# Optimization experiments

Measured on AMD Instinct MI355X. Metric: run time of the kernel, lower is better.

## Reference

```python
import jax, jax.numpy as jnp
import numpy as np

NEMBED, EMBED_DIM, HID_DIM, OUT_DIM, NUM_CLASSES = 128, 64, 128, 128, 2
BATCH, TEAM = 2048, 5
N_OPS = 8


def setup_inputs() -> dict:
    key = jax.random.key(0)
    ks = jax.random.split(key, 8)
    w_eq = np.sqrt(2.0 / (EMBED_DIM + HID_DIM + N_OPS))
    return {
        "x": jax.random.randint(ks[0], (BATCH, 2, TEAM), 0, NEMBED, dtype=jnp.int32),
        "embed": jax.random.normal(ks[1], (NEMBED, EMBED_DIM), jnp.float32) * 0.1,
        "coefs1": jax.random.normal(ks[2], (EMBED_DIM, HID_DIM, N_OPS), jnp.float32) * w_eq,
        "bias1": jnp.zeros((HID_DIM,), jnp.float32),
        "wout1": jax.random.normal(ks[3], (HID_DIM, OUT_DIM), jnp.float32) * np.sqrt(1.0 / HID_DIM),
        "bout1": jnp.zeros((OUT_DIM,), jnp.float32),
        "coefs2": jax.random.normal(ks[4], (EMBED_DIM, HID_DIM, N_OPS), jnp.float32) * w_eq,
        "bias2": jnp.zeros((HID_DIM,), jnp.float32),
        "wout2": jax.random.normal(ks[5], (HID_DIM, OUT_DIM), jnp.float32) * np.sqrt(1.0 / HID_DIM),
        "bout2": jnp.zeros((OUT_DIM,), jnp.float32),
        "fcw": jax.random.normal(ks[6], (2 * OUT_DIM, NCLS := NUM_CLASSES and 2 * OUT_DIM and NUM_CLASSES), jnp.float32) * np.sqrt(1.0 / (2 * OUT_DIM)),
        "fcb": jnp.zeros((NUM_CLASSES,), jnp.float32),
    }


def eset_ops_3_to_3(t):
    # t: (N, D, m, m, m). 8 equivariant basis ops: keep-or-(sum&broadcast) each axis.
    # Pooled ops are kept with singleton dims; broadcasting happens after the
    # channel contraction (cheaper, same math as expand-then-contract).
    s1 = t.sum(-3, keepdims=True)
    s2 = t.sum(-2, keepdims=True)
    s3 = t.sum(-1, keepdims=True)
    s12 = t.sum((-3, -2), keepdims=True)
    s13 = t.sum((-3, -1), keepdims=True)
    s23 = t.sum((-2, -1), keepdims=True)
    sall = t.sum((-3, -2, -1), keepdims=True)
    return [t, s1, s2, s3, s12, s13, s23, sall]


def eq3_layer(t, coefs, bias):
    # coefs: (D_in, D_out, 8); output (N, D_out, m, m, m)
    ops = eset_ops_3_to_3(t)
    out = 0.0
    for b, op in enumerate(ops):
        out = out + jnp.einsum('ndijk,ds->nsijk', op, coefs[:, :, b])
    return out + bias[None, :, None, None, None]


def setnet3to3(t, coefs, bias, wout, bout):
    h = jax.nn.relu(eq3_layer(t, coefs, bias))          # (N, H, m, m, m)
    return jnp.einsum('nsijk,so->nijko', h, wout) + bout  # (N, m, m, m, out_dim)


def reference(x, embed, coefs1, bias1, wout1, bout1, coefs2, bias2, wout2, bout2, fcw, fcb):
    e1 = jax.nn.relu(embed[x[:, 0]])  # (N, 5, D)
    e2 = jax.nn.relu(embed[x[:, 1]])
    t1 = jnp.einsum('bid,bjd,bkd->bdijk', e1, e1, e1)  # (N, D, 5, 5, 5)
    t2 = jnp.einsum('bid,bjd,bkd->bdijk', e2, e2, e2)
    o1 = setnet3to3(t1, coefs1, bias1, wout1, bout1)
    o2 = setnet3to3(t2, coefs2, bias2, wout2, bout2)
    t1e = jax.nn.relu(o1.mean(axis=(1, 2, 3)))  # (N, out_dim)
    t2e = jax.nn.relu(o2.mean(axis=(1, 2, 3)))
    z = jnp.concatenate([t1e, t2e], axis=-1)    # dropout_prob=0 / eval mode: no-op
    return z @ fcw + fcb
```

## Files before the change

### kernel.cpp

```cpp
#include <hip/hip_runtime.h>


typedef __attribute__((ext_vector_type(8))) short bf16x8;
typedef __attribute__((ext_vector_type(4))) float f32x4;
typedef __attribute__((ext_vector_type(4))) unsigned u32x4;

#define DEV __device__ __forceinline__
#define MFMA __builtin_amdgcn_mfma_f32_16x16x32_bf16

DEV constexpr int pid2(int a, int b) {
  int x = a < b ? a : b, y = a < b ? b : a;
  return x * (9 - x) / 2 + y;
}
DEV constexpr int tid3(int i, int j, int k) {
  int a = i, b = j, c = k, t;
  if (a > b) { t = a; a = b; b = t; }
  if (b > c) { t = b; b = c; c = t; }
  if (a > b) { t = a; a = b; b = t; }
  return a * (a * a - 18 * a + 107) / 6 + (b - a) * (11 - a - b) / 2 + (c - b);
}
DEV ushort f2bf(float f) {
  unsigned u = __builtin_bit_cast(unsigned, f);
  return (ushort)((u + 0x7FFFu + ((u >> 16) & 1u)) >> 16);
}
DEV unsigned pk2(float a, float b) {
  return (unsigned)f2bf(a) | ((unsigned)f2bf(b) << 16);
}

__global__ __launch_bounds__(256)
void prep_kernel(const float* __restrict__ c1, const float* __restrict__ c2,
                 const float* __restrict__ w1, const float* __restrict__ w2,
                 ushort* __restrict__ ctf, float* __restrict__ wt, int do_wt) {
  const int idx = blockIdx.x * 256 + threadIdx.x;
  if (idx < 131072) {
    const int e = idx & 7, l = (idx >> 3) & 63, nt = (idx >> 9) & 7,
              kt = (idx >> 12) & 1, bank = (idx >> 13) & 7, side = (idx >> 16) & 1;
    const int d = 32 * kt + 8 * (l >> 4) + e;
    const int s = 16 * nt + (l & 15);
    ctf[idx] = f2bf((side ? c2 : c1)[(d * 128 + s) * 8 + bank]);
  } else if (do_wt) {
    const int j = idx - 131072;
    if (j < 65536) {
      const int s = j & 127, o = (j >> 7) & 127, side = j >> 14;
      wt[j] = (side ? w2 : w1)[s * 128 + o] * (1.f / 125.f);
    }
  }
}

__global__ __launch_bounds__(256, 3)
void eq3_wavegemm(const int* __restrict__ x, const float* __restrict__ embed,
                  const float* __restrict__ bias1, const float* __restrict__ bias2,
                  const float* __restrict__ bout1, const float* __restrict__ bout2,
                  const float* __restrict__ wout1, const float* __restrict__ wout2,
                  const float* __restrict__ fcw,
                  const ushort* __restrict__ ctf, const float* __restrict__ wt,
                  float* __restrict__ pbuf, int nunits)
{
  __shared__ ushort FT[80 * 64];
  __shared__ ushort TS[8 * 2184];
  __shared__ float  S2[256];
  __shared__ float  SW[256];
  __shared__ float  fcp[4];

  const int tid = threadIdx.x;
  const int w = tid >> 6, l = tid & 63, grp = l >> 4, lc = l & 15;

  for (int e = tid; e < 24 * 64; e += 256) {
    const int r = e >> 6, d = e & 63;
    const int row = (r < 13) ? 35 + r : ((r == 13) ? 63 : 70 + (r - 14));
    FT[(row * 64 + d) ^ ((row & 7) << 3)] = 0;
  }
  int uprev = -1;

  for (int u = blockIdx.x; u < nunits; u += gridDim.x) {
    const int side = u & 1;

    {
      const int d = tid & 63, q = tid >> 6;
      const int* xn = x + u * 5;
      float v[5];
      #pragma unroll
      for (int i = 0; i < 5; ++i) v[i] = fmaxf(embed[xn[i] * 64 + d], 0.f);
      const float Sv = v[0] + v[1] + v[2] + v[3] + v[4];
      const float Sq = Sv * Sv, Sc = Sq * Sv;
      float p2a[15];
      {
        int c2 = 0;
        #pragma unroll
        for (int a = 0; a < 5; ++a)
          #pragma unroll
          for (int b = a; b < 5; ++b) { p2a[c2] = v[a] * v[b]; ++c2; }
      }
      {
        int c3 = 0;
        #pragma unroll
        for (int a = 0; a < 5; ++a)
          #pragma unroll
          for (int b = a; b < 5; ++b)
            #pragma unroll
            for (int c = b; c < 5; ++c) {
              const int qq = (c3 < 14) ? 0 : ((c3 < 28) ? 1 : 2);
              if (q == qq)
                FT[(c3 * 64 + d) ^ ((c3 & 7) << 3)] = f2bf(p2a[pid2(a, b)] * v[c]);
              ++c3;
            }
      }
      #pragma unroll
      for (int p = 0; p < 15; ++p) {
        const int qq = (p < 7) ? 2 : 3;
        const int row = 48 + p;
        if (q == qq) FT[(row * 64 + d) ^ ((row & 7) << 3)] = f2bf(Sv * p2a[p]);
      }
      if (q == 3) {
        #pragma unroll
        for (int i = 0; i < 5; ++i) {
          const int row = 64 + i;
          FT[(row * 64 + d) ^ ((row & 7) << 3)] = f2bf(Sq * v[i]);
        }
        FT[(69 * 64 + d) ^ ((69 & 7) << 3)] = f2bf(Sc);
      }
    }
    __syncthreads();

    if (uprev >= 0 && tid == 0) {
      pbuf[2 * uprev]     = fcp[0] + fcp[2];
      pbuf[2 * uprev + 1] = fcp[1] + fcp[3];
    }

    {
      const ushort* cbase = ctf + side * 65536;
      #pragma unroll
      for (int sub = 0; sub < 2; ++sub) {
        const int nti = 2 * w + sub;
        auto FR = [&](int t0, int kt) -> bf16x8 {
          const int t = t0 + lc;
          return *(const bf16x8*)(FT + ((t * 64 + 32 * kt + 8 * grp) ^ ((t & 7) << 3)));
        };
        auto CR = [&](int bank, int kt) -> bf16x8 {
          return *(const bf16x8*)(cbase + (((bank * 2 + kt) * 8 + nti) * 64 + l) * 8);
        };
        ushort* tb = TS + nti * 2184 + lc * 136;
        f32x4 a;
        a = {0.f, 0.f, 0.f, 0.f};
        a = MFMA(FR(0, 0), CR(0, 0), a, 0, 0, 0);
        a = MFMA(FR(0, 1), CR(0, 1), a, 0, 0, 0);
        { uint2 t2; t2.x = pk2(a[0], a[1]); t2.y = pk2(a[2], a[3]);
          *reinterpret_cast<uint2*>(tb + 4 * grp) = t2; }
        a = {0.f, 0.f, 0.f, 0.f};
        a = MFMA(FR(16, 0), CR(0, 0), a, 0, 0, 0);
        a = MFMA(FR(16, 1), CR(0, 1), a, 0, 0, 0);
        { uint2 t2; t2.x = pk2(a[0], a[1]); t2.y = pk2(a[2], a[3]);
          *reinterpret_cast<uint2*>(tb + 16 + 4 * grp) = t2; }
        a = {0.f, 0.f, 0.f, 0.f};
        a = MFMA(FR(32, 0), CR(0, 0), a, 0, 0, 0);
        a = MFMA(FR(32, 1), CR(0, 1), a, 0, 0, 0);
        if (grp == 0) {
          *reinterpret_cast<unsigned*>(tb + 32) = pk2(a[0], a[1]);
          tb[34] = f2bf(a[2]);
        }
        {
          const bf16x8 A0 = FR(48, 0), A1 = FR(48, 1);
          #pragma unroll
          for (int bk = 1; bk <= 3; ++bk) {
            const int cb = 48 + 16 * (bk - 1);
            a = {0.f, 0.f, 0.f, 0.f};
            a = MFMA(A0, CR(bk, 0), a, 0, 0, 0);
            a = MFMA(A1, CR(bk, 1), a, 0, 0, 0);
            if (grp < 3) {
              uint2 t2; t2.x = pk2(a[0], a[1]); t2.y = pk2(a[2], a[3]);
              *reinterpret_cast<uint2*>(tb + cb + 4 * grp) = t2;
            } else {
              *reinterpret_cast<unsigned*>(tb + cb + 12) = pk2(a[0], a[1]);
              tb[cb + 14] = f2bf(a[2]);
            }
          }
        }
        {
          const bf16x8 A0 = FR(64, 0), A1 = FR(64, 1);
          #pragma unroll
          for (int bk = 4; bk <= 6; ++bk) {
            const int cb = 96 + 8 * (bk - 4);
            a = {0.f, 0.f, 0.f, 0.f};
            a = MFMA(A0, CR(bk, 0), a, 0, 0, 0);
            a = MFMA(A1, CR(bk, 1), a, 0, 0, 0);
            if (grp == 0) {
              uint2 t2; t2.x = pk2(a[0], a[1]); t2.y = pk2(a[2], a[3]);
              *reinterpret_cast<uint2*>(tb + cb) = t2;
            } else if (grp == 1) {
              tb[cb + 4] = f2bf(a[0]);
            }
          }
          a = {0.f, 0.f, 0.f, 0.f};
          a = MFMA(A0, CR(7, 0), a, 0, 0, 0);
          a = MFMA(A1, CR(7, 1), a, 0, 0, 0);
          if (grp == 1) tb[120] = f2bf(a[1]);
        }
      }
    }
    __syncthreads();

    {
      const int ch = tid & 127, half = tid >> 7;
      const ushort* trow = TS + (ch >> 4) * 2184 + (ch & 15) * 136;
      u32x4 R[16];
      #pragma unroll
      for (int j = 0; j < 16; ++j) R[j] = *(const u32x4*)(trow + 8 * j);
      __builtin_amdgcn_sched_barrier(0);
      auto ext = [&](int c) -> float {
        const unsigned wv = R[c >> 3][(c >> 1) & 3];
        return __builtin_bit_cast(float, (c & 1) ? (wv & 0xFFFF0000u) : (wv << 16));
      };
      const float* bi = side ? bias2 : bias1;
      const float base = ext(120) + bi[ch];
      float hs = 0.f;
      #define CELLK(i, j, k)                                                      \
        hs += fmaxf(pij + ext(96 + (k)) + ext(64 + pid2(i, k)) +                  \
                    ext(48 + pid2(j, k)) + ext(tid3(i, j, k)), 0.f);
      if (half == 0) {
        #pragma unroll
        for (int i = 0; i < 2; ++i) {
          const float pi = base + ext(112 + i);
          #pragma unroll
          for (int j = 0; j < 5; ++j) {
            const float pij = pi + ext(104 + j) + ext(80 + pid2(i, j));
            #pragma unroll
            for (int k = 0; k < 5; ++k) CELLK(i, j, k)
          }
        }
        {
          const float pi = base + ext(112 + 2);
          #pragma unroll
          for (int j = 0; j < 2; ++j) {
            const float pij = pi + ext(104 + j) + ext(80 + pid2(2, j));
            #pragma unroll
            for (int k = 0; k < 5; ++k) CELLK(2, j, k)
          }
          {
            const float pij = pi + ext(104 + 2) + ext(80 + pid2(2, 2));
            #pragma unroll
            for (int k = 0; k < 3; ++k) CELLK(2, 2, k)
          }
        }
      } else {
        {
          const float pi = base + ext(112 + 2);
          {
            const float pij = pi + ext(104 + 2) + ext(80 + pid2(2, 2));
            #pragma unroll
            for (int k = 3; k < 5; ++k) CELLK(2, 2, k)
          }
          #pragma unroll
          for (int j = 3; j < 5; ++j) {
            const float pij = pi + ext(104 + j) + ext(80 + pid2(2, j));
            #pragma unroll
            for (int k = 0; k < 5; ++k) CELLK(2, j, k)
          }
        }
        #pragma unroll
        for (int i = 3; i < 5; ++i) {
          const float pi = base + ext(112 + i);
          #pragma unroll
          for (int j = 0; j < 5; ++j) {
            const float pij = pi + ext(104 + j) + ext(80 + pid2(i, j));
            #pragma unroll
            for (int k = 0; k < 5; ++k) CELLK(i, j, k)
          }
        }
      }
      #undef CELLK
      S2[half * 128 + ch] = hs;
    }
    __syncthreads();

    {
      const int o = tid & 127, h = tid >> 7;
      float r;
      if (wt != nullptr) {
        const f32x4* wv = (const f32x4*)(wt + side * 16384 + o * 128 + h * 64);
        const f32x4* pa = (const f32x4*)(S2 + h * 64);
        const f32x4* pb = (const f32x4*)(S2 + 128 + h * 64);
        float a0 = 0.f, a1 = 0.f, a2 = 0.f, a3 = 0.f;
        #pragma unroll
        for (int q2 = 0; q2 < 16; ++q2) {
          const f32x4 hq = pa[q2] + pb[q2];
          const f32x4 wq = wv[q2];
          a0 = fmaf(hq[0], wq[0], a0);
          a1 = fmaf(hq[1], wq[1], a1);
          a2 = fmaf(hq[2], wq[2], a2);
          a3 = fmaf(hq[3], wq[3], a3);
        }
        r = (a0 + a1) + (a2 + a3);
      } else {
        const float* W = side ? wout2 : wout1;
        float acc = 0.f;
        #pragma unroll 8
        for (int s = 64 * h; s < 64 * h + 64; ++s)
          acc = fmaf((S2[s] + S2[128 + s]) * (1.f / 125.f), W[s * 128 + o], acc);
        r = acc;
      }
      SW[h * 128 + o] = r;
    }
    __syncthreads();

    if (tid < 128) {
      const int o = tid;
      const float* bo = side ? bout2 : bout1;
      const float z = fmaxf(SW[o] + SW[128 + o] + bo[o], 0.f);
      const float* fw = fcw + side * 256;
      float p0 = z * fw[2 * o], p1 = z * fw[2 * o + 1];
      #pragma unroll
      for (int off = 32; off; off >>= 1) {
        p0 += __shfl_down(p0, off);
        p1 += __shfl_down(p1, off);
      }
      if ((tid & 63) == 0) { fcp[(tid >> 6) * 2] = p0; fcp[(tid >> 6) * 2 + 1] = p1; }
    }
    uprev = u;
  }

  if (uprev >= 0) {
    __syncthreads();
    if (tid == 0) {
      pbuf[2 * uprev]     = fcp[0] + fcp[2];
      pbuf[2 * uprev + 1] = fcp[1] + fcp[3];
    }
  }
}

__global__ __launch_bounds__(256)
void fc_final(const float* __restrict__ pbuf, const float* __restrict__ fcb,
              float* __restrict__ out, int nout) {
  const int t = blockIdx.x * 256 + threadIdx.x;
  if (t < nout) {
    const int n = t >> 1, c = t & 1;
    out[t] = pbuf[4 * n + c] + pbuf[4 * n + 2 + c] + fcb[c];
  }
}

extern "C" void kernel_launch(void* const* d_in, const int* in_sizes, int n_in,
                              void* d_out, int out_size, void* d_ws, size_t ws_size,
                              hipStream_t stream) {
  const int*   x      = (const int*)  d_in[0];
  const float* embed  = (const float*)d_in[1];
  const float* coefs1 = (const float*)d_in[2];
  const float* bias1  = (const float*)d_in[3];
  const float* wout1  = (const float*)d_in[4];
  const float* bout1  = (const float*)d_in[5];
  const float* coefs2 = (const float*)d_in[6];
  const float* bias2  = (const float*)d_in[7];
  const float* wout2  = (const float*)d_in[8];
  const float* bout2  = (const float*)d_in[9];
  const float* fcw    = (const float*)d_in[10];
  const float* fcb    = (const float*)d_in[11];
  float* out = (float*)d_out;

  float*  pbuf = (float*)d_ws;
  ushort* ctf  = (ushort*)((char*)d_ws + 32768);
  const int do_wt = (ws_size >= (size_t)(32768 + 262144 + 131072)) ? 1 : 0;
  float*  wt   = do_wt ? (float*)((char*)d_ws + 32768 + 262144) : nullptr;

  const int batch  = in_sizes[0] / 10;
  const int nunits = batch * 2;

  prep_kernel<<<768, 256, 0, stream>>>(coefs1, coefs2, wout1, wout2, ctf, wt, do_wt);
  eq3_wavegemm<<<768, 256, 0, stream>>>(
      x, embed, bias1, bias2, bout1, bout2, wout1, wout2, fcw, ctf, wt, pbuf, nunits);
  fc_final<<<(nunits + 255) / 256, 256, 0, stream>>>(pbuf, fcb, out, nunits);
}
```

Before: 85.59 us.

## Compute 125-cell pooled-term gather-sum with MFMA using 0/1 selection matrix

Replaces the per-thread scalar expansion of the 125 output cells (summing pooled/unique terms from TS then ReLU) with MFMA products of a constant 0/1 bf16 selection matrix against the TS rows. The selection fragments are built once per block in LDS and kept in registers; bias is written into TS column 121 so the MFMA also adds it. Each wave covers two 16-cell tiles, reduces ReLU outputs with shuffles, and S2 grows to four partial slices. This moves VALU gather/adds onto matrix cores at the cost of extra registers (32 VGPRs of fragments) and accumulation in a bf16-input MFMA rather than fp32 adds.

```diff
diff --git a/kernel.cpp b/kernel.cpp
--- a/kernel.cpp
+++ b/kernel.cpp
@@ -3,7 +3,6 @@
 
 typedef __attribute__((ext_vector_type(8))) short bf16x8;
 typedef __attribute__((ext_vector_type(4))) float f32x4;
-typedef __attribute__((ext_vector_type(4))) unsigned u32x4;
 
 #define DEV __device__ __forceinline__
 #define MFMA __builtin_amdgcn_mfma_f32_16x16x32_bf16
@@ -58,7 +57,8 @@
 {
   __shared__ ushort FT[80 * 64];
   __shared__ ushort TS[8 * 2184];
-  __shared__ float  S2[256];
+  __shared__ unsigned char MB[2048];
+  __shared__ float  S2[512];
   __shared__ float  SW[256];
   __shared__ float  fcp[4];
 
@@ -70,6 +70,38 @@
     const int row = (r < 13) ? 35 + r : ((r == 13) ? 63 : 70 + (r - 14));
     FT[(row * 64 + d) ^ ((row & 7) << 3)] = 0;
   }
+  for (int e = tid; e < 8736; e += 256) ((unsigned*)TS)[e] = 0;
+  for (int idx = tid; idx < 2048; idx += 256) {
+    const int mt = idx >> 8, kt = (idx >> 6) & 3, ll = idx & 63;
+    const int cell = 16 * mt + (ll & 15);
+    const int seg = 4 * kt + (ll >> 4);
+    unsigned by = 0;
+    if (cell < 125) {
+      const int i = cell / 25, rm = cell - 25 * i, j = rm / 5, k = rm - 5 * j;
+      const int tv[9] = { tid3(i, j, k), 48 + pid2(j, k), 64 + pid2(i, k),
+                          80 + pid2(i, j), 96 + k, 104 + j, 112 + i, 120, 121 };
+      #pragma unroll
+      for (int e = 0; e < 9; ++e)
+        if ((tv[e] >> 3) == seg) by |= 1u << (tv[e] & 7);
+    }
+    MB[idx] = (unsigned char)by;
+  }
+  __syncthreads();
+
+  bf16x8 af[2][4];
+  #pragma unroll
+  for (int m = 0; m < 2; ++m)
+    #pragma unroll
+    for (int kt = 0; kt < 4; ++kt) {
+      const unsigned by = MB[((2 * w + m) * 4 + kt) * 64 + l];
+      unsigned fr[4];
+      #pragma unroll
+      for (int qd = 0; qd < 4; ++qd)
+        fr[qd] = (((by >> (2 * qd)) & 1u) * 0x3F80u) |
+                 (((by >> (2 * qd + 1)) & 1u) * 0x3F800000u);
+      af[m][kt] = __builtin_bit_cast(bf16x8, *(const bf16x8*)fr);
+    }
+
   int uprev = -1;
 
   for (int u = blockIdx.x; u < nunits; u += gridDim.x) {
@@ -118,6 +150,10 @@
           FT[(row * 64 + d) ^ ((row & 7) << 3)] = f2bf(Sq * v[i]);
         }
         FT[(69 * 64 + d) ^ ((69 & 7) << 3)] = f2bf(Sc);
+      }
+      if (tid < 128) {
+        const float* bi = side ? bias2 : bias1;
+        TS[(tid >> 4) * 2184 + (tid & 15) * 136 + 121] = f2bf(bi[tid]);
       }
     }
     __syncthreads();
@@ -200,75 +236,25 @@
     __syncthreads();
 
     {
-      const int ch = tid & 127, half = tid >> 7;
-      const ushort* trow = TS + (ch >> 4) * 2184 + (ch & 15) * 136;
-      u32x4 R[16];
-      #pragma unroll
-      for (int j = 0; j < 16; ++j) R[j] = *(const u32x4*)(trow + 8 * j);
-      __builtin_amdgcn_sched_barrier(0);
-      auto ext = [&](int c) -> float {
-        const unsigned wv = R[c >> 3][(c >> 1) & 3];
-        return __builtin_bit_cast(float, (c & 1) ? (wv & 0xFFFF0000u) : (wv << 16));
-      };
-      const float* bi = side ? bias2 : bias1;
-      const float base = ext(120) + bi[ch];
-      float hs = 0.f;
-      #define CELLK(i, j, k)                                                      \
-        hs += fmaxf(pij + ext(96 + (k)) + ext(64 + pid2(i, k)) +                  \
-                    ext(48 + pid2(j, k)) + ext(tid3(i, j, k)), 0.f);
-      if (half == 0) {
-        #pragma unroll
-        for (int i = 0; i < 2; ++i) {
-          const float pi = base + ext(112 + i);
-          #pragma unroll
-          for (int j = 0; j < 5; ++j) {
-            const float pij = pi + ext(104 + j) + ext(80 + pid2(i, j));
-            #pragma unroll
-            for (int k = 0; k < 5; ++k) CELLK(i, j, k)
-          }
-        }
-        {
-          const float pi = base + ext(112 + 2);
-          #pragma unroll
-          for (int j = 0; j < 2; ++j) {
-            const float pij = pi + ext(104 + j) + ext(80 + pid2(2, j));
-            #pragma unroll
-            for (int k = 0; k < 5; ++k) CELLK(2, j, k)
-          }
-          {
-            const float pij = pi + ext(104 + 2) + ext(80 + pid2(2, 2));
-            #pragma unroll
-            for (int k = 0; k < 3; ++k) CELLK(2, 2, k)
-          }
-        }
-      } else {
-        {
-          const float pi = base + ext(112 + 2);
-          {
-            const float pij = pi + ext(104 + 2) + ext(80 + pid2(2, 2));
-            #pragma unroll
-            for (int k = 3; k < 5; ++k) CELLK(2, 2, k)
-          }
-          #pragma unroll
-          for (int j = 3; j < 5; ++j) {
-            const float pij = pi + ext(104 + j) + ext(80 + pid2(2, j));
-            #pragma unroll
-            for (int k = 0; k < 5; ++k) CELLK(2, j, k)
-          }
-        }
-        #pragma unroll
-        for (int i = 3; i < 5; ++i) {
-          const float pi = base + ext(112 + i);
-          #pragma unroll
-          for (int j = 0; j < 5; ++j) {
-            const float pij = pi + ext(104 + j) + ext(80 + pid2(i, j));
-            #pragma unroll
-            for (int k = 0; k < 5; ++k) CELLK(i, j, k)
-          }
-        }
-      }
-      #undef CELLK
-      S2[half * 128 + ch] = hs;
+      #pragma unroll
+      for (int nt = 0; nt < 8; ++nt) {
+        const ushort* tb = TS + nt * 2184 + lc * 136;
+        f32x4 a0 = {0.f, 0.f, 0.f, 0.f};
+        f32x4 a1 = {0.f, 0.f, 0.f, 0.f};
+        #pragma unroll
+        for (int kt = 0; kt < 4; ++kt) {
+          const bf16x8 Bf = *(const bf16x8*)(tb + 32 * kt + 8 * grp);
+          a0 = MFMA(af[0][kt], Bf, a0, 0, 0, 0);
+          a1 = MFMA(af[1][kt], Bf, a1, 0, 0, 0);
+        }
+        float hs = fmaxf(a0[0], 0.f) + fmaxf(a0[1], 0.f)
+                 + fmaxf(a0[2], 0.f) + fmaxf(a0[3], 0.f)
+                 + fmaxf(a1[0], 0.f) + fmaxf(a1[1], 0.f)
+                 + fmaxf(a1[2], 0.f) + fmaxf(a1[3], 0.f);
+        hs += __shfl_xor(hs, 16);
+        hs += __shfl_xor(hs, 32);
+        if (l < 16) S2[w * 128 + 16 * nt + lc] = hs;
+      }
     }
     __syncthreads();
 
@@ -279,10 +265,12 @@
         const f32x4* wv = (const f32x4*)(wt + side * 16384 + o * 128 + h * 64);
         const f32x4* pa = (const f32x4*)(S2 + h * 64);
         const f32x4* pb = (const f32x4*)(S2 + 128 + h * 64);
+        const f32x4* pc = (const f32x4*)(S2 + 256 + h * 64);
+        const f32x4* pd = (const f32x4*)(S2 + 384 + h * 64);
         float a0 = 0.f, a1 = 0.f, a2 = 0.f, a3 = 0.f;
         #pragma unroll
         for (int q2 = 0; q2 < 16; ++q2) {
-          const f32x4 hq = pa[q2] + pb[q2];
+          const f32x4 hq = (pa[q2] + pb[q2]) + (pc[q2] + pd[q2]);
           const f32x4 wq = wv[q2];
           a0 = fmaf(hq[0], wq[0], a0);
           a1 = fmaf(hq[1], wq[1], a1);
@@ -295,7 +283,8 @@
         float acc = 0.f;
         #pragma unroll 8
         for (int s = 64 * h; s < 64 * h + 64; ++s)
-          acc = fmaf((S2[s] + S2[128 + s]) * (1.f / 125.f), W[s * 128 + o], acc);
+          acc = fmaf((S2[s] + S2[128 + s] + S2[256 + s] + S2[384 + s]) * (1.f / 125.f),
+                     W[s * 128 + o], acc);
         r = acc;
       }
       SW[h * 128 + o] = r;
```

Measured after the change: 146.2 us. 70.8% more time.

## Software-pipeline phases across units to cut barriers per iteration

Applied to the files above, without the earlier changes.

Restructures the persistent per-block loop into a two-stage software pipeline. The feature build and MFMA GEMM for the next unit are interleaved with the assembly, Wout and FC phases of the current unit, so each iteration needs two barriers instead of four. Side-dependent pointers are hoisted, which relies on the grid size being even so a block always stays on the same side. Buffer reuse between phases must stay race-free, and register pressure may rise from interleaving.

```diff
diff --git a/kernel.cpp b/kernel.cpp
--- a/kernel.cpp
+++ b/kernel.cpp
@@ -48,13 +48,13 @@
 }
 
 __global__ __launch_bounds__(256, 3)
-void eq3_wavegemm(const int* __restrict__ x, const float* __restrict__ embed,
-                  const float* __restrict__ bias1, const float* __restrict__ bias2,
-                  const float* __restrict__ bout1, const float* __restrict__ bout2,
-                  const float* __restrict__ wout1, const float* __restrict__ wout2,
-                  const float* __restrict__ fcw,
-                  const ushort* __restrict__ ctf, const float* __restrict__ wt,
-                  float* __restrict__ pbuf, int nunits)
+void eq3_pipe(const int* __restrict__ x, const float* __restrict__ embed,
+              const float* __restrict__ bias1, const float* __restrict__ bias2,
+              const float* __restrict__ bout1, const float* __restrict__ bout2,
+              const float* __restrict__ wout1, const float* __restrict__ wout2,
+              const float* __restrict__ fcw,
+              const ushort* __restrict__ ctf, const float* __restrict__ wt,
+              float* __restrict__ pbuf, int nunits)
 {
   __shared__ ushort FT[80 * 64];
   __shared__ ushort TS[8 * 2184];
@@ -65,265 +65,279 @@
   const int tid = threadIdx.x;
   const int w = tid >> 6, l = tid & 63, grp = l >> 4, lc = l & 15;
 
+  const int side = blockIdx.x & 1;
+  const float*  bi    = side ? bias2 : bias1;
+  const float*  bo    = side ? bout2 : bout1;
+  const float*  Wf    = side ? wout2 : wout1;
+  const float*  fw    = fcw + side * 256;
+  const ushort* cbase = ctf + side * 65536;
+
+  int ucur = blockIdx.x;
+  if (ucur >= nunits) return;
+
   for (int e = tid; e < 24 * 64; e += 256) {
     const int r = e >> 6, d = e & 63;
     const int row = (r < 13) ? 35 + r : ((r == 13) ? 63 : 70 + (r - 14));
     FT[(row * 64 + d) ^ ((row & 7) << 3)] = 0;
   }
+
+  auto phaseA = [&](int u) {
+    const int d = tid & 63, q = tid >> 6;
+    const int* xn = x + u * 5;
+    float v[5];
+    #pragma unroll
+    for (int i = 0; i < 5; ++i) v[i] = fmaxf(embed[xn[i] * 64 + d], 0.f);
+    const float Sv = v[0] + v[1] + v[2] + v[3] + v[4];
+    const float Sq = Sv * Sv, Sc = Sq * Sv;
+    float p2a[15];
+    {
+      int c2 = 0;
+      #pragma unroll
+      for (int a = 0; a < 5; ++a)
+        #pragma unroll
+        for (int b = a; b < 5; ++b) { p2a[c2] = v[a] * v[b]; ++c2; }
+    }
+    {
+      int c3 = 0;
+      #pragma unroll
+      for (int a = 0; a < 5; ++a)
+        #pragma unroll
+        for (int b = a; b < 5; ++b)
+          #pragma unroll
+          for (int c = b; c < 5; ++c) {
+            const int qq = (c3 < 14) ? 0 : ((c3 < 28) ? 1 : 2);
+            if (q == qq)
+              FT[(c3 * 64 + d) ^ ((c3 & 7) << 3)] = f2bf(p2a[pid2(a, b)] * v[c]);
+            ++c3;
+          }
+    }
+    #pragma unroll
+    for (int p = 0; p < 15; ++p) {
+      const int qq = (p < 7) ? 2 : 3;
+      const int row = 48 + p;
+      if (q == qq) FT[(row * 64 + d) ^ ((row & 7) << 3)] = f2bf(Sv * p2a[p]);
+    }
+    if (q == 3) {
+      #pragma unroll
+      for (int i = 0; i < 5; ++i) {
+        const int row = 64 + i;
+        FT[(row * 64 + d) ^ ((row & 7) << 3)] = f2bf(Sq * v[i]);
+      }
+      FT[(69 * 64 + d) ^ ((69 & 7) << 3)] = f2bf(Sc);
+    }
+  };
+
+  auto phaseG1 = [&]() {
+    #pragma unroll
+    for (int sub = 0; sub < 2; ++sub) {
+      const int nti = 2 * w + sub;
+      auto FR = [&](int t0, int kt) -> bf16x8 {
+        const int t = t0 + lc;
+        return *(const bf16x8*)(FT + ((t * 64 + 32 * kt + 8 * grp) ^ ((t & 7) << 3)));
+      };
+      auto CR = [&](int bank, int kt) -> bf16x8 {
+        return *(const bf16x8*)(cbase + (((bank * 2 + kt) * 8 + nti) * 64 + l) * 8);
+      };
+      ushort* tb = TS + nti * 2184 + lc * 136;
+      f32x4 a;
+      a = {0.f, 0.f, 0.f, 0.f};
+      a = MFMA(FR(0, 0), CR(0, 0), a, 0, 0, 0);
+      a = MFMA(FR(0, 1), CR(0, 1), a, 0, 0, 0);
+      { uint2 t2; t2.x = pk2(a[0], a[1]); t2.y = pk2(a[2], a[3]);
+        *reinterpret_cast<uint2*>(tb + 4 * grp) = t2; }
+      a = {0.f, 0.f, 0.f, 0.f};
+      a = MFMA(FR(16, 0), CR(0, 0), a, 0, 0, 0);
+      a = MFMA(FR(16, 1), CR(0, 1), a, 0, 0, 0);
+      { uint2 t2; t2.x = pk2(a[0], a[1]); t2.y = pk2(a[2], a[3]);
+        *reinterpret_cast<uint2*>(tb + 16 + 4 * grp) = t2; }
+      a = {0.f, 0.f, 0.f, 0.f};
+      a = MFMA(FR(32, 0), CR(0, 0), a, 0, 0, 0);
+      a = MFMA(FR(32, 1), CR(0, 1), a, 0, 0, 0);
+      if (grp == 0) {
+        *reinterpret_cast<unsigned*>(tb + 32) = pk2(a[0], a[1]);
+        tb[34] = f2bf(a[2]);
+      }
+      {
+        const bf16x8 A0 = FR(48, 0), A1 = FR(48, 1);
+        #pragma unroll
+        for (int bk = 1; bk <= 3; ++bk) {
+          const int cb = 48 + 16 * (bk - 1);
+          a = {0.f, 0.f, 0.f, 0.f};
+          a = MFMA(A0, CR(bk, 0), a, 0, 0, 0);
+          a = MFMA(A1, CR(bk, 1), a, 0, 0, 0);
+          if (grp < 3) {
+            uint2 t2; t2.x = pk2(a[0], a[1]); t2.y = pk2(a[2], a[3]);
+            *reinterpret_cast<uint2*>(tb + cb + 4 * grp) = t2;
+          } else {
+            *reinterpret_cast<unsigned*>(tb + cb + 12) = pk2(a[0], a[1]);
+            tb[cb + 14] = f2bf(a[2]);
+          }
+        }
+      }
+      {
+        const bf16x8 A0 = FR(64, 0), A1 = FR(64, 1);
+        #pragma unroll
+        for (int bk = 4; bk <= 6; ++bk) {
+          const int cb = 96 + 8 * (bk - 4);
+          a = {0.f, 0.f, 0.f, 0.f};
+          a = MFMA(A0, CR(bk, 0), a, 0, 0, 0);
+          a = MFMA(A1, CR(bk, 1), a, 0, 0, 0);
+          if (grp == 0) {
+            uint2 t2; t2.x = pk2(a[0], a[1]); t2.y = pk2(a[2], a[3]);
+            *reinterpret_cast<uint2*>(tb + cb) = t2;
+          } else if (grp == 1) {
+            tb[cb + 4] = f2bf(a[0]);
+          }
+        }
+        a = {0.f, 0.f, 0.f, 0.f};
+        a = MFMA(A0, CR(7, 0), a, 0, 0, 0);
+        a = MFMA(A1, CR(7, 1), a, 0, 0, 0);
+        if (grp == 1) tb[120] = f2bf(a[1]);
+      }
+    }
+  };
+
+  auto phaseAsm = [&]() {
+    const int ch = tid & 127, half = tid >> 7;
+    const ushort* trow = TS + (ch >> 4) * 2184 + (ch & 15) * 136;
+    u32x4 R[16];
+    #pragma unroll
+    for (int j = 0; j < 16; ++j) R[j] = *(const u32x4*)(trow + 8 * j);
+    __builtin_amdgcn_sched_barrier(0);
+    auto ext = [&](int c) -> float {
+      const unsigned wv = R[c >> 3][(c >> 1) & 3];
+      return __builtin_bit_cast(float, (c & 1) ? (wv & 0xFFFF0000u) : (wv << 16));
+    };
+    const float base = ext(120) + bi[ch];
+    float hs = 0.f;
+    #define CELLK(i, j, k)                                                      \
+      hs += fmaxf(pij + ext(96 + (k)) + ext(64 + pid2(i, k)) +                  \
+                  ext(48 + pid2(j, k)) + ext(tid3(i, j, k)), 0.f);
+    if (half == 0) {
+      #pragma unroll
+      for (int i = 0; i < 2; ++i) {
+        const float pi = base + ext(112 + i);
+        #pragma unroll
+        for (int j = 0; j < 5; ++j) {
+          const float pij = pi + ext(104 + j) + ext(80 + pid2(i, j));
+          #pragma unroll
+          for (int k = 0; k < 5; ++k) CELLK(i, j, k)
+        }
+      }
+      {
+        const float pi = base + ext(112 + 2);
+        #pragma unroll
+        for (int j = 0; j < 2; ++j) {
+          const float pij = pi + ext(104 + j) + ext(80 + pid2(2, j));
+          #pragma unroll
+          for (int k = 0; k < 5; ++k) CELLK(2, j, k)
+        }
+        {
+          const float pij = pi + ext(104 + 2) + ext(80 + pid2(2, 2));
+          #pragma unroll
+          for (int k = 0; k < 3; ++k) CELLK(2, 2, k)
+        }
+      }
+    } else {
+      {
+        const float pi = base + ext(112 + 2);
+        {
+          const float pij = pi + ext(104 + 2) + ext(80 + pid2(2, 2));
+          #pragma unroll
+          for (int k = 3; k < 5; ++k) CELLK(2, 2, k)
+        }
+        #pragma unroll
+        for (int j = 3; j < 5; ++j) {
+          const float pij = pi + ext(104 + j) + ext(80 + pid2(2, j));
+          #pragma unroll
+          for (int k = 0; k < 5; ++k) CELLK(2, j, k)
+        }
+      }
+      #pragma unroll
+      for (int i = 3; i < 5; ++i) {
+        const float pi = base + ext(112 + i);
+        #pragma unroll
+        for (int j = 0; j < 5; ++j) {
+          const float pij = pi + ext(104 + j) + ext(80 + pid2(i, j));
+          #pragma unroll
+          for (int k = 0; k < 5; ++k) CELLK(i, j, k)
+        }
+      }
+    }
+    #undef CELLK
+    S2[half * 128 + ch] = hs;
+  };
+
+  auto phaseWout = [&]() {
+    const int o = tid & 127, h = tid >> 7;
+    float r;
+    if (wt != nullptr) {
+      const f32x4* wv = (const f32x4*)(wt + side * 16384 + o * 128 + h * 64);
+      const f32x4* pa = (const f32x4*)(S2 + h * 64);
+      const f32x4* pb = (const f32x4*)(S2 + 128 + h * 64);
+      float a0 = 0.f, a1 = 0.f, a2 = 0.f, a3 = 0.f;
+      #pragma unroll
+      for (int q2 = 0; q2 < 16; ++q2) {
+        const f32x4 hq = pa[q2] + pb[q2];
+        const f32x4 wq = wv[q2];
+        a0 = fmaf(hq[0], wq[0], a0);
+        a1 = fmaf(hq[1], wq[1], a1);
+        a2 = fmaf(hq[2], wq[2], a2);
+        a3 = fmaf(hq[3], wq[3], a3);
+      }
+      r = (a0 + a1) + (a2 + a3);
+    } else {
+      float acc = 0.f;
+      #pragma unroll 8
+      for (int s = 64 * h; s < 64 * h + 64; ++s)
+        acc = fmaf((S2[s] + S2[128 + s]) * (1.f / 125.f), Wf[s * 128 + o], acc);
+      r = acc;
+    }
+    SW[h * 128 + o] = r;
+  };
+
+  auto phaseZFC = [&]() {
+    if (tid < 128) {
+      const int o = tid;
+      const float z = fmaxf(SW[o] + SW[128 + o] + bo[o], 0.f);
+      float p0 = z * fw[2 * o], p1 = z * fw[2 * o + 1];
+      #pragma unroll
+      for (int off = 32; off; off >>= 1) {
+        p0 += __shfl_down(p0, off);
+        p1 += __shfl_down(p1, off);
+      }
+      if ((tid & 63) == 0) { fcp[(tid >> 6) * 2] = p0; fcp[(tid >> 6) * 2 + 1] = p1; }
+    }
+  };
+
+  phaseA(ucur);
+  __syncthreads();
+  phaseG1();
+  __syncthreads();
   int uprev = -1;
-
-  for (int u = blockIdx.x; u < nunits; u += gridDim.x) {
-    const int side = u & 1;
-
-    {
-      const int d = tid & 63, q = tid >> 6;
-      const int* xn = x + u * 5;
-      float v[5];
-      #pragma unroll
-      for (int i = 0; i < 5; ++i) v[i] = fmaxf(embed[xn[i] * 64 + d], 0.f);
-      const float Sv = v[0] + v[1] + v[2] + v[3] + v[4];
-      const float Sq = Sv * Sv, Sc = Sq * Sv;
-      float p2a[15];
-      {
-        int c2 = 0;
-        #pragma unroll
-        for (int a = 0; a < 5; ++a)
-          #pragma unroll
-          for (int b = a; b < 5; ++b) { p2a[c2] = v[a] * v[b]; ++c2; }
-      }
-      {
-        int c3 = 0;
-        #pragma unroll
-        for (int a = 0; a < 5; ++a)
-          #pragma unroll
-          for (int b = a; b < 5; ++b)
-            #pragma unroll
-            for (int c = b; c < 5; ++c) {
-              const int qq = (c3 < 14) ? 0 : ((c3 < 28) ? 1 : 2);
-              if (q == qq)
-                FT[(c3 * 64 + d) ^ ((c3 & 7) << 3)] = f2bf(p2a[pid2(a, b)] * v[c]);
-              ++c3;
-            }
-      }
-      #pragma unroll
-      for (int p = 0; p < 15; ++p) {
-        const int qq = (p < 7) ? 2 : 3;
-        const int row = 48 + p;
-        if (q == qq) FT[(row * 64 + d) ^ ((row & 7) << 3)] = f2bf(Sv * p2a[p]);
-      }
-      if (q == 3) {
-        #pragma unroll
-        for (int i = 0; i < 5; ++i) {
-          const int row = 64 + i;
-          FT[(row * 64 + d) ^ ((row & 7) << 3)] = f2bf(Sq * v[i]);
-        }
-        FT[(69 * 64 + d) ^ ((69 & 7) << 3)] = f2bf(Sc);
-      }
-    }
+  while (true) {
+    const int unext = ucur + gridDim.x;
+    const bool hn = unext < nunits;
+    if (uprev >= 0) phaseZFC();
+    phaseAsm();
+    if (hn) phaseA(unext);
     __syncthreads();
-
     if (uprev >= 0 && tid == 0) {
       pbuf[2 * uprev]     = fcp[0] + fcp[2];
       pbuf[2 * uprev + 1] = fcp[1] + fcp[3];
     }
-
-    {
-      const ushort* cbase = ctf + side * 65536;
-      #pragma unroll
-      for (int sub = 0; sub < 2; ++sub) {
-        const int nti = 2 * w + sub;
-        auto FR = [&](int t0, int kt) -> bf16x8 {
-          const int t = t0 + lc;
-          return *(const bf16x8*)(FT + ((t * 64 + 32 * kt + 8 * grp) ^ ((t & 7) << 3)));
-        };
-        auto CR = [&](int bank, int kt) -> bf16x8 {
-          return *(const bf16x8*)(cbase + (((bank * 2 + kt) * 8 + nti) * 64 + l) * 8);
-        };
-        ushort* tb = TS + nti * 2184 + lc * 136;
-        f32x4 a;
-        a = {0.f, 0.f, 0.f, 0.f};
-        a = MFMA(FR(0, 0), CR(0, 0), a, 0, 0, 0);
-        a = MFMA(FR(0, 1), CR(0, 1), a, 0, 0, 0);
-        { uint2 t2; t2.x = pk2(a[0], a[1]); t2.y = pk2(a[2], a[3]);
-          *reinterpret_cast<uint2*>(tb + 4 * grp) = t2; }
-        a = {0.f, 0.f, 0.f, 0.f};
-        a = MFMA(FR(16, 0), CR(0, 0), a, 0, 0, 0);
-        a = MFMA(FR(16, 1), CR(0, 1), a, 0, 0, 0);
-        { uint2 t2; t2.x = pk2(a[0], a[1]); t2.y = pk2(a[2], a[3]);
-          *reinterpret_cast<uint2*>(tb + 16 + 4 * grp) = t2; }
-        a = {0.f, 0.f, 0.f, 0.f};
-        a = MFMA(FR(32, 0), CR(0, 0), a, 0, 0, 0);
-        a = MFMA(FR(32, 1), CR(0, 1), a, 0, 0, 0);
-        if (grp == 0) {
-          *reinterpret_cast<unsigned*>(tb + 32) = pk2(a[0], a[1]);
-          tb[34] = f2bf(a[2]);
-        }
-        {
-          const bf16x8 A0 = FR(48, 0), A1 = FR(48, 1);
-          #pragma unroll
-          for (int bk = 1; bk <= 3; ++bk) {
-            const int cb = 48 + 16 * (bk - 1);
-            a = {0.f, 0.f, 0.f, 0.f};
-            a = MFMA(A0, CR(bk, 0), a, 0, 0, 0);
-            a = MFMA(A1, CR(bk, 1), a, 0, 0, 0);
-            if (grp < 3) {
-              uint2 t2; t2.x = pk2(a[0], a[1]); t2.y = pk2(a[2], a[3]);
-              *reinterpret_cast<uint2*>(tb + cb + 4 * grp) = t2;
-            } else {
-              *reinterpret_cast<unsigned*>(tb + cb + 12) = pk2(a[0], a[1]);
-              tb[cb + 14] = f2bf(a[2]);
-            }
-          }
-        }
-        {
-          const bf16x8 A0 = FR(64, 0), A1 = FR(64, 1);
-          #pragma unroll
-          for (int bk = 4; bk <= 6; ++bk) {
-            const int cb = 96 + 8 * (bk - 4);
-            a = {0.f, 0.f, 0.f, 0.f};
-            a = MFMA(A0, CR(bk, 0), a, 0, 0, 0);
-            a = MFMA(A1, CR(bk, 1), a, 0, 0, 0);
-            if (grp == 0) {
-              uint2 t2; t2.x = pk2(a[0], a[1]); t2.y = pk2(a[2], a[3]);
-              *reinterpret_cast<uint2*>(tb + cb) = t2;
-            } else if (grp == 1) {
-              tb[cb + 4] = f2bf(a[0]);
-            }
-          }
-          a = {0.f, 0.f, 0.f, 0.f};
-          a = MFMA(A0, CR(7, 0), a, 0, 0, 0);
-          a = MFMA(A1, CR(7, 1), a, 0, 0, 0);
-          if (grp == 1) tb[120] = f2bf(a[1]);
-        }
-      }
-    }
+    phaseWout();
+    if (hn) phaseG1();
     __syncthreads();
-
-    {
-      const int ch = tid & 127, half = tid >> 7;
-      const ushort* trow = TS + (ch >> 4) * 2184 + (ch & 15) * 136;
-      u32x4 R[16];
-      #pragma unroll
-      for (int j = 0; j < 16; ++j) R[j] = *(const u32x4*)(trow + 8 * j);
-      __builtin_amdgcn_sched_barrier(0);
-      auto ext = [&](int c) -> float {
-        const unsigned wv = R[c >> 3][(c >> 1) & 3];
-        return __builtin_bit_cast(float, (c & 1) ? (wv & 0xFFFF0000u) : (wv << 16));
-      };
-      const float* bi = side ? bias2 : bias1;
-      const float base = ext(120) + bi[ch];
-      float hs = 0.f;
-      #define CELLK(i, j, k)                                                      \
-        hs += fmaxf(pij + ext(96 + (k)) + ext(64 + pid2(i, k)) +                  \
-                    ext(48 + pid2(j, k)) + ext(tid3(i, j, k)), 0.f);
-      if (half == 0) {
-        #pragma unroll
-        for (int i = 0; i < 2; ++i) {
-          const float pi = base + ext(112 + i);
-          #pragma unroll
-          for (int j = 0; j < 5; ++j) {
-            const float pij = pi + ext(104 + j) + ext(80 + pid2(i, j));
-            #pragma unroll
-            for (int k = 0; k < 5; ++k) CELLK(i, j, k)
-          }
-        }
-        {
-          const float pi = base + ext(112 + 2);
-          #pragma unroll
-          for (int j = 0; j < 2; ++j) {
-            const float pij = pi + ext(104 + j) + ext(80 + pid2(2, j));
-            #pragma unroll
-            for (int k = 0; k < 5; ++k) CELLK(2, j, k)
-          }
-          {
-            const float pij = pi + ext(104 + 2) + ext(80 + pid2(2, 2));
-            #pragma unroll
-            for (int k = 0; k < 3; ++k) CELLK(2, 2, k)
-          }
-        }
-      } else {
-        {
-          const float pi = base + ext(112 + 2);
-          {
-            const float pij = pi + ext(104 + 2) + ext(80 + pid2(2, 2));
-            #pragma unroll
-            for (int k = 3; k < 5; ++k) CELLK(2, 2, k)
-          }
-          #pragma unroll
-          for (int j = 3; j < 5; ++j) {
-            const float pij = pi + ext(104 + j) + ext(80 + pid2(2, j));
-            #pragma unroll
-            for (int k = 0; k < 5; ++k) CELLK(2, j, k)
-          }
-        }
-        #pragma unroll
-        for (int i = 3; i < 5; ++i) {
-          const float pi = base + ext(112 + i);
-          #pragma unroll
-          for (int j = 0; j < 5; ++j) {
-            const float pij = pi + ext(104 + j) + ext(80 + pid2(i, j));
-            #pragma unroll
-            for (int k = 0; k < 5; ++k) CELLK(i, j, k)
-          }
-        }
-      }
-      #undef CELLK
-      S2[half * 128 + ch] = hs;
-    }
-    __syncthreads();
-
-    {
-      const int o = tid & 127, h = tid >> 7;
-      float r;
-      if (wt != nullptr) {
-        const f32x4* wv = (const f32x4*)(wt + side * 16384 + o * 128 + h * 64);
-        const f32x4* pa = (const f32x4*)(S2 + h * 64);
-        const f32x4* pb = (const f32x4*)(S2 + 128 + h * 64);
-        float a0 = 0.f, a1 = 0.f, a2 = 0.f, a3 = 0.f;
-        #pragma unroll
-        for (int q2 = 0; q2 < 16; ++q2) {
-          const f32x4 hq = pa[q2] + pb[q2];
-          const f32x4 wq = wv[q2];
-          a0 = fmaf(hq[0], wq[0], a0);
-          a1 = fmaf(hq[1], wq[1], a1);
-          a2 = fmaf(hq[2], wq[2], a2);
-          a3 = fmaf(hq[3], wq[3], a3);
-        }
-        r = (a0 + a1) + (a2 + a3);
-      } else {
-        const float* W = side ? wout2 : wout1;
-        float acc = 0.f;
-        #pragma unroll 8
-        for (int s = 64 * h; s < 64 * h + 64; ++s)
-          acc = fmaf((S2[s] + S2[128 + s]) * (1.f / 125.f), W[s * 128 + o], acc);
-        r = acc;
-      }
-      SW[h * 128 + o] = r;
-    }
-    __syncthreads();
-
-    if (tid < 128) {
-      const int o = tid;
-      const float* bo = side ? bout2 : bout1;
-      const float z = fmaxf(SW[o] + SW[128 + o] + bo[o], 0.f);
-      const float* fw = fcw + side * 256;
-      float p0 = z * fw[2 * o], p1 = z * fw[2 * o + 1];
-      #pragma unroll
-      for (int off = 32; off; off >>= 1) {
-        p0 += __shfl_down(p0, off);
-        p1 += __shfl_down(p1, off);
-      }
-      if ((tid & 63) == 0) { fcp[(tid >> 6) * 2] = p0; fcp[(tid >> 6) * 2 + 1] = p1; }
-    }
-    uprev = u;
-  }
-
-  if (uprev >= 0) {
-    __syncthreads();
-    if (tid == 0) {
-      pbuf[2 * uprev]     = fcp[0] + fcp[2];
-      pbuf[2 * uprev + 1] = fcp[1] + fcp[3];
-    }
+    uprev = ucur;
+    if (!hn) break;
+    ucur = unext;
+  }
+  phaseZFC();
+  __syncthreads();
+  if (tid == 0) {
+    pbuf[2 * uprev]     = fcp[0] + fcp[2];
+    pbuf[2 * uprev + 1] = fcp[1] + fcp[3];
   }
 }
 
@@ -363,7 +377,7 @@
   const int nunits = batch * 2;
 
   prep_kernel<<<768, 256, 0, stream>>>(coefs1, coefs2, wout1, wout2, ctf, wt, do_wt);
-  eq3_wavegemm<<<768, 256, 0, stream>>>(
+  eq3_pipe<<<768, 256, 0, stream>>>(
       x, embed, bias1, bias2, bout1, bout2, wout1, wout2, fcw, ctf, wt, pbuf, nunits);
   fc_final<<<(nunits + 255) / 256, 256, 0, stream>>>(pbuf, fcb, out, nunits);
 }
```

Result: slower. 124.9 us (+45.9%).
